# Kernel optimization log

Measured on AMD Instinct MI355X. Metric: run time of the kernel, lower is better.

Reference implementation:

```python
import jax, jax.numpy as jnp
import numpy as np

EDGE_DIM = 64
NODE_DIM = 64
HIDDEN_DIM = 256
N_EDGES = 1_000_000
N_NODES = 100_000


def setup_inputs() -> dict:
    key = jax.random.key(0)
    k_e, k_v, k_idx, k_w1, k_b1, k_w2, k_b2 = jax.random.split(key, 7)
    E = jax.random.normal(k_e, (N_EDGES, EDGE_DIM), dtype=jnp.float32)
    V = jax.random.normal(k_v, (N_NODES, NODE_DIM), dtype=jnp.float32)
    edge_index = jax.random.randint(k_idx, (2, N_EDGES), 0, N_NODES, dtype=jnp.int64)
    in_dim = EDGE_DIM + 2 * NODE_DIM  # 192
    # Kaiming-uniform-ish init like torch Linear defaults
    lim1 = 1.0 / np.sqrt(in_dim)
    lim2 = 1.0 / np.sqrt(HIDDEN_DIM)
    W1 = jax.random.uniform(k_w1, (in_dim, HIDDEN_DIM), jnp.float32, -lim1, lim1)
    b1 = jax.random.uniform(k_b1, (HIDDEN_DIM,), jnp.float32, -lim1, lim1)
    W2 = jax.random.uniform(k_w2, (HIDDEN_DIM, HIDDEN_DIM), jnp.float32, -lim2, lim2)
    b2 = jax.random.uniform(k_b2, (HIDDEN_DIM,), jnp.float32, -lim2, lim2)
    return {"E": E, "V": V, "edge_index": edge_index,
            "W1": W1, "b1": b1, "W2": W2, "b2": b2}


def reference(E, V, edge_index, W1, b1, W2, b2):
    src = edge_index[0]
    dst = edge_index[1]
    v_src = V[src]                       # [N_e, F_v] gather
    v_dst = V[dst]                       # [N_e, F_v] gather
    x = jnp.concatenate([E, v_src, v_dst], axis=-1)  # [N_e, F_e + 2*F_v]
    h = jax.nn.relu(x @ W1 + b1)         # [N_e, hidden]
    return h @ W2 + b2                   # [N_e, hidden]
```

## Files before the change

### kernel.cpp

```cpp
#include <hip/hip_runtime.h>
#include <hip/hip_bf16.h>

#define N_EDGES_C 1000000
#define EDGE_DIM_C 64
#define NODE_DIM_C 64
#define IN_DIM_C   192
#define HID_C      256
#define XPAD 200
#define HS_OFF 25600
#define T_TILES 5

typedef __attribute__((ext_vector_type(8))) short  short8;
typedef __attribute__((ext_vector_type(4))) float  f32x4;

#define BAR_LDS() asm volatile("s_waitcnt lgkmcnt(0)\n\ts_barrier" ::: "memory")

__device__ __forceinline__ unsigned short f2bf(float f) {
    union { float f; unsigned u; } v; v.f = f;
    unsigned u = v.u;
    u += 0x7fffu + ((u >> 16) & 1u);
    return (unsigned short)(u >> 16);
}

__global__ void prep_weights_kernel(const float* __restrict__ W1,
                                    const float* __restrict__ W2,
                                    unsigned short* __restrict__ W1T,
                                    unsigned short* __restrict__ W2T) {
    int tid = blockIdx.x * 256 + threadIdx.x;
    if (tid < IN_DIM_C * HID_C) {
        int n = tid / IN_DIM_C, k = tid - n * IN_DIM_C;
        W1T[tid] = f2bf(W1[k * HID_C + n]);
    } else {
        int t2 = tid - IN_DIM_C * HID_C;
        if (t2 < HID_C * HID_C) {
            int o = t2 / HID_C, k = t2 - o * HID_C;
            W2T[t2] = f2bf(W2[k * HID_C + o]);
        }
    }
}

__global__ __launch_bounds__(512, 2) void edge_mlp_kernel(
    const float* __restrict__ E, const float* __restrict__ V,
    const int* __restrict__ srcI, const int* __restrict__ dstI,
    const unsigned short* __restrict__ W1T, const float* __restrict__ b1,
    const unsigned short* __restrict__ W2T, const float* __restrict__ b2,
    float* __restrict__ out)
{
    __shared__ unsigned char smem[HS_OFF + 32768];
    unsigned short* Xs = (unsigned short*)smem;

    const int tid = threadIdx.x;
    const int w  = tid >> 6;
    const int l  = tid & 63;
    const int lm = l & 15;
    const int lg = l >> 4;
    const long block0 = (long)blockIdx.x * (64 * T_TILES);

    short8 wA1[6][2];
    short8 wA2[8][2];
#pragma unroll
    for (int kb = 0; kb < 6; ++kb)
#pragma unroll
        for (int nt = 0; nt < 2; ++nt)
            wA1[kb][nt] = *reinterpret_cast<const short8*>(
                W1T + (size_t)(w * 32 + nt * 16 + lm) * IN_DIM_C + kb * 32 + lg * 8);
#pragma unroll
    for (int kb = 0; kb < 8; ++kb)
#pragma unroll
        for (int ot = 0; ot < 2; ++ot)
            wA2[kb][ot] = *reinterpret_cast<const short8*>(
                W2T + (size_t)(w * 32 + ot * 16 + lm) * HID_C + kb * 32 + lg * 8);

    float4 fE[2];
    float4 fV[4];

    auto issue = [&](long tb) {
        int kind = (l >> 3) & 1;
        int rr   = l & 7;
        const int* ip = kind ? dstI : srcI;
        int myidx = ip[tb + w * 8 + rr];
#pragma unroll
        for (int i = 0; i < 2; ++i) {
            int f = i * 64 + l;
            fE[i] = *reinterpret_cast<const float4*>(
                E + (size_t)(tb + w * 8 + (f >> 4)) * EDGE_DIM_C + (f & 15) * 4);
        }
#pragma unroll
        for (int i = 0; i < 4; ++i) {
            int kind2 = ((l & 31) < 16) ? 0 : 1;
            int srcl  = kind2 * 8 + i * 2 + (l >> 5);
            int gi = __builtin_amdgcn_ds_bpermute(srcl << 2, myidx);
            fV[i] = *reinterpret_cast<const float4*>(
                V + (size_t)gi * NODE_DIM_C + (l & 15) * 4);
        }
    };

    auto write_lds = [&]() {
#pragma unroll
        for (int i = 0; i < 2; ++i) {
            int f = i * 64 + l;
            ushort4 b;
            b.x = f2bf(fE[i].x); b.y = f2bf(fE[i].y);
            b.z = f2bf(fE[i].z); b.w = f2bf(fE[i].w);
            *reinterpret_cast<ushort4*>(
                &Xs[(w * 8 + (f >> 4)) * XPAD + (f & 15) * 4]) = b;
        }
#pragma unroll
        for (int i = 0; i < 4; ++i) {
            int kind2 = ((l & 31) < 16) ? 0 : 1;
            int rV    = i * 2 + (l >> 5);
            ushort4 b;
            b.x = f2bf(fV[i].x); b.y = f2bf(fV[i].y);
            b.z = f2bf(fV[i].z); b.w = f2bf(fV[i].w);
            *reinterpret_cast<ushort4*>(
                &Xs[(w * 8 + rV) * XPAD + 64 + kind2 * 64 + (l & 15) * 4]) = b;
        }
    };

    issue(block0);
    write_lds();
    BAR_LDS();

#pragma unroll 1
    for (int t = 0; t < T_TILES; ++t) {
        const long tb = block0 + t * 64;
        if (t + 1 < T_TILES) issue(tb + 64);

        f32x4 acc[2][4];
#pragma unroll
        for (int a = 0; a < 2; ++a)
#pragma unroll
            for (int b = 0; b < 4; ++b)
                acc[a][b] = (f32x4){0.f, 0.f, 0.f, 0.f};

#pragma unroll
        for (int kb = 0; kb < 6; ++kb) {
            short8 bx[4];
#pragma unroll
            for (int mt = 0; mt < 4; ++mt)
                bx[mt] = *reinterpret_cast<const short8*>(
                    &Xs[(mt * 16 + lm) * XPAD + kb * 32 + lg * 8]);
#pragma unroll
            for (int nt = 0; nt < 2; ++nt)
#pragma unroll
                for (int mt = 0; mt < 4; ++mt)
                    acc[nt][mt] = __builtin_amdgcn_mfma_f32_16x16x32_bf16(
                        wA1[kb][nt], bx[mt], acc[nt][mt], 0, 0, 0);
        }
        BAR_LDS();

        if (t + 1 < T_TILES) write_lds();

#pragma unroll
        for (int nt = 0; nt < 2; ++nt) {
            int n0 = w * 32 + nt * 16 + lg * 4;
            float4 bv = *reinterpret_cast<const float4*>(b1 + n0);
#pragma unroll
            for (int mt = 0; mt < 4; ++mt) {
                f32x4 a = acc[nt][mt];
                ushort4 hb;
                hb.x = f2bf(fmaxf(a[0] + bv.x, 0.f));
                hb.y = f2bf(fmaxf(a[1] + bv.y, 0.f));
                hb.z = f2bf(fmaxf(a[2] + bv.z, 0.f));
                hb.w = f2bf(fmaxf(a[3] + bv.w, 0.f));
                int m = mt * 16 + lm;
                int addr = m * 512 + ((n0 * 2) ^ (lm << 4));
                *reinterpret_cast<ushort4*>(smem + HS_OFF + addr) = hb;
            }
        }
        BAR_LDS();

#pragma unroll
        for (int a = 0; a < 2; ++a)
#pragma unroll
            for (int b = 0; b < 4; ++b)
                acc[a][b] = (f32x4){0.f, 0.f, 0.f, 0.f};

#pragma unroll
        for (int kb = 0; kb < 8; ++kb) {
            short8 bh[4];
#pragma unroll
            for (int mt = 0; mt < 4; ++mt) {
                int m = mt * 16 + lm;
                int addr = m * 512 + (((kb * 32 + lg * 8) * 2) ^ (lm << 4));
                bh[mt] = *reinterpret_cast<const short8*>(smem + HS_OFF + addr);
            }
#pragma unroll
            for (int ot = 0; ot < 2; ++ot)
#pragma unroll
                for (int mt = 0; mt < 4; ++mt)
                    acc[ot][mt] = __builtin_amdgcn_mfma_f32_16x16x32_bf16(
                        wA2[kb][ot], bh[mt], acc[ot][mt], 0, 0, 0);
        }

#pragma unroll
        for (int ot = 0; ot < 2; ++ot) {
            int o0 = w * 32 + ot * 16 + lg * 4;
            float4 bv = *reinterpret_cast<const float4*>(b2 + o0);
#pragma unroll
            for (int mt = 0; mt < 4; ++mt) {
                f32x4 a = acc[ot][mt];
                f32x4 r;
                r[0] = a[0] + bv.x;
                r[1] = a[1] + bv.y;
                r[2] = a[2] + bv.z;
                r[3] = a[3] + bv.w;
                __builtin_nontemporal_store(r, reinterpret_cast<f32x4*>(
                    out + (size_t)(tb + mt * 16 + lm) * HID_C + o0));
            }
        }
    }
}

extern "C" void kernel_launch(void* const* d_in, const int* in_sizes, int n_in,
                              void* d_out, int out_size, void* d_ws, size_t ws_size,
                              hipStream_t stream) {
    const float* E  = (const float*)d_in[0];
    const float* V  = (const float*)d_in[1];
    const int*   ei = (const int*)d_in[2];
    const float* W1 = (const float*)d_in[3];
    const float* b1 = (const float*)d_in[4];
    const float* W2 = (const float*)d_in[5];
    const float* b2 = (const float*)d_in[6];
    float* out = (float*)d_out;

    unsigned short* W1T = (unsigned short*)d_ws;
    unsigned short* W2T = W1T + IN_DIM_C * HID_C;

    const int prep_total = IN_DIM_C * HID_C + HID_C * HID_C;
    prep_weights_kernel<<<(prep_total + 255) / 256, 256, 0, stream>>>(W1, W2, W1T, W2T);

    const int nblocks = N_EDGES_C / (64 * T_TILES);
    edge_mlp_kernel<<<nblocks, 512, 0, stream>>>(
        E, V, ei, ei + N_EDGES_C, W1T, b1, W2T, b2, out);
}
```

Baseline: 511.1 us.

## Stream weights from cache per k-step and shrink blocks to 256 threads, 32-edge tiles

```diff
diff --git a/kernel.cpp b/kernel.cpp
--- a/kernel.cpp
+++ b/kernel.cpp
@@ -7,8 +7,8 @@
 #define IN_DIM_C   192
 #define HID_C      256
 #define XPAD 200
-#define HS_OFF 25600
-#define T_TILES 5
+#define HS_OFF 12800
+#define T_TILES 10
 
 typedef __attribute__((ext_vector_type(8))) short  short8;
 typedef __attribute__((ext_vector_type(4))) float  f32x4;
@@ -39,14 +39,14 @@
     }
 }
 
-__global__ __launch_bounds__(512, 2) void edge_mlp_kernel(
+__global__ __launch_bounds__(256, 3) void edge_mlp_kernel(
     const float* __restrict__ E, const float* __restrict__ V,
     const int* __restrict__ srcI, const int* __restrict__ dstI,
     const unsigned short* __restrict__ W1T, const float* __restrict__ b1,
     const unsigned short* __restrict__ W2T, const float* __restrict__ b2,
     float* __restrict__ out)
 {
-    __shared__ unsigned char smem[HS_OFF + 32768];
+    __shared__ unsigned char smem[HS_OFF + 16384];
     unsigned short* Xs = (unsigned short*)smem;
 
     const int tid = threadIdx.x;
@@ -54,109 +54,114 @@
     const int l  = tid & 63;
     const int lm = l & 15;
     const int lg = l >> 4;
-    const long block0 = (long)blockIdx.x * (64 * T_TILES);
-
-    short8 wA1[6][2];
-    short8 wA2[8][2];
-#pragma unroll
-    for (int kb = 0; kb < 6; ++kb)
-#pragma unroll
-        for (int nt = 0; nt < 2; ++nt)
-            wA1[kb][nt] = *reinterpret_cast<const short8*>(
-                W1T + (size_t)(w * 32 + nt * 16 + lm) * IN_DIM_C + kb * 32 + lg * 8);
-#pragma unroll
-    for (int kb = 0; kb < 8; ++kb)
-#pragma unroll
-        for (int ot = 0; ot < 2; ++ot)
-            wA2[kb][ot] = *reinterpret_cast<const short8*>(
-                W2T + (size_t)(w * 32 + ot * 16 + lm) * HID_C + kb * 32 + lg * 8);
+    const int r0 = tid >> 4;
+    const long block0 = (long)blockIdx.x * (32 * T_TILES);
 
     float4 fE[2];
     float4 fV[4];
-
-    auto issue = [&](long tb) {
-        int kind = (l >> 3) & 1;
-        int rr   = l & 7;
-        const int* ip = kind ? dstI : srcI;
-        int myidx = ip[tb + w * 8 + rr];
+    int idxN[4];
+
+    auto load_idx = [&](long tb) {
+        idxN[0] = srcI[tb + r0];
+        idxN[1] = srcI[tb + r0 + 16];
+        idxN[2] = dstI[tb + r0];
+        idxN[3] = dstI[tb + r0 + 16];
+    };
+
+    auto issueEV = [&](long tb, const int* idx) {
 #pragma unroll
         for (int i = 0; i < 2; ++i) {
-            int f = i * 64 + l;
+            int f = tid + i * 256;
             fE[i] = *reinterpret_cast<const float4*>(
-                E + (size_t)(tb + w * 8 + (f >> 4)) * EDGE_DIM_C + (f & 15) * 4);
-        }
-#pragma unroll
-        for (int i = 0; i < 4; ++i) {
-            int kind2 = ((l & 31) < 16) ? 0 : 1;
-            int srcl  = kind2 * 8 + i * 2 + (l >> 5);
-            int gi = __builtin_amdgcn_ds_bpermute(srcl << 2, myidx);
+                E + (size_t)(tb + (f >> 4)) * EDGE_DIM_C + (f & 15) * 4);
+        }
+#pragma unroll
+        for (int i = 0; i < 4; ++i)
             fV[i] = *reinterpret_cast<const float4*>(
-                V + (size_t)gi * NODE_DIM_C + (l & 15) * 4);
-        }
+                V + (size_t)idx[i] * NODE_DIM_C + (tid & 15) * 4);
     };
 
     auto write_lds = [&]() {
 #pragma unroll
         for (int i = 0; i < 2; ++i) {
-            int f = i * 64 + l;
+            int f = tid + i * 256;
             ushort4 b;
             b.x = f2bf(fE[i].x); b.y = f2bf(fE[i].y);
             b.z = f2bf(fE[i].z); b.w = f2bf(fE[i].w);
             *reinterpret_cast<ushort4*>(
-                &Xs[(w * 8 + (f >> 4)) * XPAD + (f & 15) * 4]) = b;
+                &Xs[(f >> 4) * XPAD + (f & 15) * 4]) = b;
         }
 #pragma unroll
         for (int i = 0; i < 4; ++i) {
-            int kind2 = ((l & 31) < 16) ? 0 : 1;
-            int rV    = i * 2 + (l >> 5);
+            int r   = (i & 1) * 16 + r0;
+            int off = 64 + (i >> 1) * 64;
             ushort4 b;
             b.x = f2bf(fV[i].x); b.y = f2bf(fV[i].y);
             b.z = f2bf(fV[i].z); b.w = f2bf(fV[i].w);
             *reinterpret_cast<ushort4*>(
-                &Xs[(w * 8 + rV) * XPAD + 64 + kind2 * 64 + (l & 15) * 4]) = b;
+                &Xs[r * XPAD + off + (tid & 15) * 4]) = b;
         }
     };
 
-    issue(block0);
-    write_lds();
+    {
+        int idx0[4];
+        idx0[0] = srcI[block0 + r0];
+        idx0[1] = srcI[block0 + r0 + 16];
+        idx0[2] = dstI[block0 + r0];
+        idx0[3] = dstI[block0 + r0 + 16];
+        issueEV(block0, idx0);
+        write_lds();
+        if (T_TILES > 1) load_idx(block0 + 32);
+    }
     BAR_LDS();
 
 #pragma unroll 1
     for (int t = 0; t < T_TILES; ++t) {
-        const long tb = block0 + t * 64;
-        if (t + 1 < T_TILES) issue(tb + 64);
-
-        f32x4 acc[2][4];
-#pragma unroll
-        for (int a = 0; a < 2; ++a)
-#pragma unroll
-            for (int b = 0; b < 4; ++b)
+        const long tb = block0 + (long)t * 32;
+        int idxC[4];
+        if (t + 1 < T_TILES) {
+#pragma unroll
+            for (int i = 0; i < 4; ++i) idxC[i] = idxN[i];
+            issueEV(tb + 32, idxC);
+            if (t + 2 < T_TILES) load_idx(tb + 64);
+        }
+
+        f32x4 acc[4][2];
+#pragma unroll
+        for (int a = 0; a < 4; ++a)
+#pragma unroll
+            for (int b = 0; b < 2; ++b)
                 acc[a][b] = (f32x4){0.f, 0.f, 0.f, 0.f};
 
+        const unsigned short* w1base = W1T + (size_t)(w * 64) * IN_DIM_C;
 #pragma unroll
         for (int kb = 0; kb < 6; ++kb) {
-            short8 bx[4];
-#pragma unroll
-            for (int mt = 0; mt < 4; ++mt)
+            short8 aw[4], bx[2];
+#pragma unroll
+            for (int nt = 0; nt < 4; ++nt)
+                aw[nt] = *reinterpret_cast<const short8*>(
+                    w1base + (size_t)(nt * 16 + lm) * IN_DIM_C + kb * 32 + lg * 8);
+#pragma unroll
+            for (int mt = 0; mt < 2; ++mt)
                 bx[mt] = *reinterpret_cast<const short8*>(
                     &Xs[(mt * 16 + lm) * XPAD + kb * 32 + lg * 8]);
 #pragma unroll
-            for (int nt = 0; nt < 2; ++nt)
-#pragma unroll
-                for (int mt = 0; mt < 4; ++mt)
+            for (int nt = 0; nt < 4; ++nt)
+#pragma unroll
+                for (int mt = 0; mt < 2; ++mt)
                     acc[nt][mt] = __builtin_amdgcn_mfma_f32_16x16x32_bf16(
-                        wA1[kb][nt], bx[mt], acc[nt][mt], 0, 0, 0);
+                        aw[nt], bx[mt], acc[nt][mt], 0, 0, 0);
         }
         BAR_LDS();
 
         if (t + 1 < T_TILES) write_lds();
 
 #pragma unroll
-        for (int nt = 0; nt < 2; ++nt) {
-            int n0 = w * 32 + nt * 16 + lg * 4;
+        for (int nt = 0; nt < 4; ++nt) {
+            int n0 = w * 64 + nt * 16 + lg * 4;
             float4 bv = *reinterpret_cast<const float4*>(b1 + n0);
 #pragma unroll
-            for (int mt = 0; mt < 4; ++mt) {
+            for (int mt = 0; mt < 2; ++mt) {
                 f32x4 a = acc[nt][mt];
                 ushort4 hb;
                 hb.x = f2bf(fmaxf(a[0] + bv.x, 0.f));
@@ -171,34 +176,39 @@
         BAR_LDS();
 
 #pragma unroll
-        for (int a = 0; a < 2; ++a)
-#pragma unroll
-            for (int b = 0; b < 4; ++b)
+        for (int a = 0; a < 4; ++a)
+#pragma unroll
+            for (int b = 0; b < 2; ++b)
                 acc[a][b] = (f32x4){0.f, 0.f, 0.f, 0.f};
 
+        const unsigned short* w2base = W2T + (size_t)(w * 64) * HID_C;
 #pragma unroll
         for (int kb = 0; kb < 8; ++kb) {
-            short8 bh[4];
-#pragma unroll
-            for (int mt = 0; mt < 4; ++mt) {
+            short8 aw[4], bh[2];
+#pragma unroll
+            for (int ot = 0; ot < 4; ++ot)
+                aw[ot] = *reinterpret_cast<const short8*>(
+                    w2base + (size_t)(ot * 16 + lm) * HID_C + kb * 32 + lg * 8);
+#pragma unroll
+            for (int mt = 0; mt < 2; ++mt) {
                 int m = mt * 16 + lm;
                 int addr = m * 512 + (((kb * 32 + lg * 8) * 2) ^ (lm << 4));
                 bh[mt] = *reinterpret_cast<const short8*>(smem + HS_OFF + addr);
             }
 #pragma unroll
-            for (int ot = 0; ot < 2; ++ot)
-#pragma unroll
-                for (int mt = 0; mt < 4; ++mt)
+            for (int ot = 0; ot < 4; ++ot)
+#pragma unroll
+                for (int mt = 0; mt < 2; ++mt)
                     acc[ot][mt] = __builtin_amdgcn_mfma_f32_16x16x32_bf16(
-                        wA2[kb][ot], bh[mt], acc[ot][mt], 0, 0, 0);
-        }
-
-#pragma unroll
-        for (int ot = 0; ot < 2; ++ot) {
-            int o0 = w * 32 + ot * 16 + lg * 4;
+                        aw[ot], bh[mt], acc[ot][mt], 0, 0, 0);
+        }
+
+#pragma unroll
+        for (int ot = 0; ot < 4; ++ot) {
+            int o0 = w * 64 + ot * 16 + lg * 4;
             float4 bv = *reinterpret_cast<const float4*>(b2 + o0);
 #pragma unroll
-            for (int mt = 0; mt < 4; ++mt) {
+            for (int mt = 0; mt < 2; ++mt) {
                 f32x4 a = acc[ot][mt];
                 f32x4 r;
                 r[0] = a[0] + bv.x;
@@ -230,7 +240,7 @@
     const int prep_total = IN_DIM_C * HID_C + HID_C * HID_C;
     prep_weights_kernel<<<(prep_total + 255) / 256, 256, 0, stream>>>(W1, W2, W1T, W2T);
 
-    const int nblocks = N_EDGES_C / (64 * T_TILES);
-    edge_mlp_kernel<<<nblocks, 512, 0, stream>>>(
+    const int nblocks = N_EDGES_C / (32 * T_TILES);
+    edge_mlp_kernel<<<nblocks, 256, 0, stream>>>(
         E, V, ei, ei + N_EDGES_C, W1T, b1, W2T, b2, out);
 }
```

New measurement: 1.206 ms. +135.9%, slower.

## Double-buffer X and H tiles in LDS, prefetch indices early, raise MFMA priority

Applied to the files above, without the earlier changes.

```diff
diff --git a/kernel.cpp b/kernel.cpp
--- a/kernel.cpp
+++ b/kernel.cpp
@@ -7,7 +7,9 @@
 #define IN_DIM_C   192
 #define HID_C      256
 #define XPAD 200
-#define HS_OFF 25600
+#define XBUF_SZ 25600
+#define HS_OFF  51200
+#define HBUF_SZ 32768
 #define T_TILES 5
 
 typedef __attribute__((ext_vector_type(8))) short  short8;
@@ -46,9 +48,7 @@
     const unsigned short* __restrict__ W2T, const float* __restrict__ b2,
     float* __restrict__ out)
 {
-    __shared__ unsigned char smem[HS_OFF + 32768];
-    unsigned short* Xs = (unsigned short*)smem;
-
+    __shared__ unsigned char smem[HS_OFF + 2 * HBUF_SZ];
     const int tid = threadIdx.x;
     const int w  = tid >> 6;
     const int l  = tid & 63;
@@ -71,37 +71,42 @@
             wA2[kb][ot] = *reinterpret_cast<const short8*>(
                 W2T + (size_t)(w * 32 + ot * 16 + lm) * HID_C + kb * 32 + lg * 8);
 
-    float4 fE[2];
-    float4 fV[4];
-
-    auto issue = [&](long tb) {
-        int kind = (l >> 3) & 1;
-        int rr   = l & 7;
-        const int* ip = kind ? dstI : srcI;
-        int myidx = ip[tb + w * 8 + rr];
+    f32x4 fE[2];
+    f32x4 fV[4];
+
+    const int kind = (l >> 3) & 1;
+    const int rr   = l & 7;
+    const int* const ip = kind ? dstI : srcI;
+
+    auto load_idx = [&](long tb) -> int {
+        return ip[tb + w * 8 + rr];
+    };
+
+    auto issueEV = [&](long tb, int myidx) {
 #pragma unroll
         for (int i = 0; i < 2; ++i) {
             int f = i * 64 + l;
-            fE[i] = *reinterpret_cast<const float4*>(
-                E + (size_t)(tb + w * 8 + (f >> 4)) * EDGE_DIM_C + (f & 15) * 4);
+            fE[i] = __builtin_nontemporal_load(reinterpret_cast<const f32x4*>(
+                E + (size_t)(tb + w * 8 + (f >> 4)) * EDGE_DIM_C + (f & 15) * 4));
         }
 #pragma unroll
         for (int i = 0; i < 4; ++i) {
             int kind2 = ((l & 31) < 16) ? 0 : 1;
             int srcl  = kind2 * 8 + i * 2 + (l >> 5);
             int gi = __builtin_amdgcn_ds_bpermute(srcl << 2, myidx);
-            fV[i] = *reinterpret_cast<const float4*>(
+            fV[i] = *reinterpret_cast<const f32x4*>(
                 V + (size_t)gi * NODE_DIM_C + (l & 15) * 4);
         }
     };
 
-    auto write_lds = [&]() {
+    auto write_lds = [&](int buf) {
+        unsigned short* Xs = (unsigned short*)(smem + buf * XBUF_SZ);
 #pragma unroll
         for (int i = 0; i < 2; ++i) {
             int f = i * 64 + l;
             ushort4 b;
-            b.x = f2bf(fE[i].x); b.y = f2bf(fE[i].y);
-            b.z = f2bf(fE[i].z); b.w = f2bf(fE[i].w);
+            b.x = f2bf(fE[i][0]); b.y = f2bf(fE[i][1]);
+            b.z = f2bf(fE[i][2]); b.w = f2bf(fE[i][3]);
             *reinterpret_cast<ushort4*>(
                 &Xs[(w * 8 + (f >> 4)) * XPAD + (f & 15) * 4]) = b;
         }
@@ -110,22 +115,30 @@
             int kind2 = ((l & 31) < 16) ? 0 : 1;
             int rV    = i * 2 + (l >> 5);
             ushort4 b;
-            b.x = f2bf(fV[i].x); b.y = f2bf(fV[i].y);
-            b.z = f2bf(fV[i].z); b.w = f2bf(fV[i].w);
+            b.x = f2bf(fV[i][0]); b.y = f2bf(fV[i][1]);
+            b.z = f2bf(fV[i][2]); b.w = f2bf(fV[i][3]);
             *reinterpret_cast<ushort4*>(
                 &Xs[(w * 8 + rV) * XPAD + 64 + kind2 * 64 + (l & 15) * 4]) = b;
         }
     };
 
-    issue(block0);
-    write_lds();
+    {
+        int idx0 = load_idx(block0);
+        issueEV(block0, idx0);
+        write_lds(0);
+    }
+    int idxNext = (T_TILES > 1) ? load_idx(block0 + 64) : 0;
     BAR_LDS();
 
 #pragma unroll 1
     for (int t = 0; t < T_TILES; ++t) {
-        const long tb = block0 + t * 64;
-        if (t + 1 < T_TILES) issue(tb + 64);
-
+        const long tb = block0 + (long)t * 64;
+        const int xb = t & 1;
+
+        if (t + 1 < T_TILES) issueEV(tb + 64, idxNext);
+        if (t + 2 < T_TILES) idxNext = load_idx(tb + 128);
+
+        const unsigned short* Xs = (const unsigned short*)(smem + xb * XBUF_SZ);
         f32x4 acc[2][4];
 #pragma unroll
         for (int a = 0; a < 2; ++a)
@@ -133,6 +146,7 @@
             for (int b = 0; b < 4; ++b)
                 acc[a][b] = (f32x4){0.f, 0.f, 0.f, 0.f};
 
+        __builtin_amdgcn_s_setprio(1);
 #pragma unroll
         for (int kb = 0; kb < 6; ++kb) {
             short8 bx[4];
@@ -147,10 +161,9 @@
                     acc[nt][mt] = __builtin_amdgcn_mfma_f32_16x16x32_bf16(
                         wA1[kb][nt], bx[mt], acc[nt][mt], 0, 0, 0);
         }
-        BAR_LDS();
-
-        if (t + 1 < T_TILES) write_lds();
-
+        __builtin_amdgcn_s_setprio(0);
+
+        unsigned char* Hb = smem + HS_OFF + xb * HBUF_SZ;
 #pragma unroll
         for (int nt = 0; nt < 2; ++nt) {
             int n0 = w * 32 + nt * 16 + lg * 4;
@@ -165,9 +178,12 @@
                 hb.w = f2bf(fmaxf(a[3] + bv.w, 0.f));
                 int m = mt * 16 + lm;
                 int addr = m * 512 + ((n0 * 2) ^ (lm << 4));
-                *reinterpret_cast<ushort4*>(smem + HS_OFF + addr) = hb;
+                *reinterpret_cast<ushort4*>(Hb + addr) = hb;
             }
         }
+
+        if (t + 1 < T_TILES) write_lds(xb ^ 1);
+
         BAR_LDS();
 
 #pragma unroll
@@ -176,6 +192,7 @@
             for (int b = 0; b < 4; ++b)
                 acc[a][b] = (f32x4){0.f, 0.f, 0.f, 0.f};
 
+        __builtin_amdgcn_s_setprio(1);
 #pragma unroll
         for (int kb = 0; kb < 8; ++kb) {
             short8 bh[4];
@@ -183,7 +200,7 @@
             for (int mt = 0; mt < 4; ++mt) {
                 int m = mt * 16 + lm;
                 int addr = m * 512 + (((kb * 32 + lg * 8) * 2) ^ (lm << 4));
-                bh[mt] = *reinterpret_cast<const short8*>(smem + HS_OFF + addr);
+                bh[mt] = *reinterpret_cast<const short8*>(Hb + addr);
             }
 #pragma unroll
             for (int ot = 0; ot < 2; ++ot)
@@ -192,6 +209,7 @@
                     acc[ot][mt] = __builtin_amdgcn_mfma_f32_16x16x32_bf16(
                         wA2[kb][ot], bh[mt], acc[ot][mt], 0, 0, 0);
         }
+        __builtin_amdgcn_s_setprio(0);
 
 #pragma unroll
         for (int ot = 0; ot < 2; ++ot) {
```

Result: no change. 510.0 us (-0.2%).
